# Optimization experiments

Measured on AMD Instinct MI355X. Metric: run time of the kernel, lower is better.

## Reference

```python
import jax, jax.numpy as jnp
import numpy as np

N = 50000
DIM_IN = 256
HID = 64
OUT = 32
E1 = 800000
E2 = 1600000
BN_EPS = 1e-5


def _make_edges(rng, n, e):
    row = rng.integers(0, n, size=e).astype(np.int32)
    col = rng.integers(0, n, size=e).astype(np.int32)
    # gcn_norm without self loops: val = d^{-1/2}[row] * d^{-1/2}[col]
    deg = np.bincount(row, minlength=n) + 0.0
    deg_c = np.bincount(col, minlength=n) + 0.0
    dr = 1.0 / np.sqrt(np.maximum(deg, 1.0))
    dc = 1.0 / np.sqrt(np.maximum(deg_c, 1.0))
    val = (dr[row] * dc[col]).astype(np.float32)
    return row, col, val


def setup_inputs() -> dict:
    key = jax.random.key(0)
    ks = jax.random.split(key, 4)
    rng = np.random.default_rng(0)
    e1_row, e1_col, e1_val = _make_edges(rng, N, E1)
    e2_row, e2_col, e2_val = _make_edges(rng, N, E2)
    return {
        "x": jax.random.normal(ks[0], (N, DIM_IN), dtype=jnp.float32),
        "e1_row": jnp.asarray(e1_row), "e1_col": jnp.asarray(e1_col), "e1_val": jnp.asarray(e1_val),
        "e2_row": jnp.asarray(e2_row), "e2_col": jnp.asarray(e2_col), "e2_val": jnp.asarray(e2_val),
        "W_embed": jax.random.normal(ks[1], (DIM_IN, HID), dtype=jnp.float32) * (1.0 / np.sqrt(DIM_IN)),
        "b_embed": jnp.zeros((HID,), dtype=jnp.float32),
        "bn0_gamma": jnp.ones((2 * HID,), dtype=jnp.float32),
        "bn0_beta": jnp.zeros((2 * HID,), dtype=jnp.float32),
        "bn1_gamma": jnp.ones((4 * HID,), dtype=jnp.float32),
        "bn1_beta": jnp.zeros((4 * HID,), dtype=jnp.float32),
        "W_head": jax.random.normal(ks[2], (15 * HID, OUT), dtype=jnp.float32) * (1.0 / np.sqrt(15 * HID)),
        "b_head": jnp.zeros((OUT,), dtype=jnp.float32),
    }


def _spmm(row, col, val, x, n):
    # out[row] += val * x[col]  (sparse [n,n] @ dense [n,d])
    return jax.ops.segment_sum(val[:, None] * x[col], row, num_segments=n)


def _bn(v, gamma, beta):
    # BatchNorm1d training-mode math: per-feature mean / biased var over nodes
    m = jnp.mean(v, axis=0)
    var = jnp.mean(jnp.square(v - m), axis=0)
    return gamma * (v - m) * jax.lax.rsqrt(var + BN_EPS) + beta


def reference(x, e1_row, e1_col, e1_val, e2_row, e2_col, e2_val,
              W_embed, b_embed, bn0_gamma, bn0_beta, bn1_gamma, bn1_beta,
              W_head, b_head):
    n = x.shape[0]

    def conv(h):
        h1 = _spmm(e1_row, e1_col, e1_val, h, n)
        h2 = _spmm(e2_row, e2_col, e2_val, h, n)
        return jnp.concatenate([h1, h2], axis=1)

    h = jax.nn.relu(x @ W_embed + b_embed)          # [n, HID]
    xs = [h]
    c0 = _bn(conv(h), bn0_gamma, bn0_beta)           # [n, 2*HID]
    xs.append(c0)
    c1 = _bn(conv(c0), bn1_gamma, bn1_beta)          # [n, 4*HID]
    xs.append(c1)
    c2 = conv(c1)                                    # [n, 8*HID]
    xs.append(c2)
    j = jnp.concatenate(xs, axis=1)                  # [n, 15*HID]
    return j @ W_head + b_head                       # [n, OUT]
```

## Files before the change

### kernel.cpp

```cpp
#include <hip/hip_runtime.h>


#define NN  50000
#define E1N 800000
#define E2N 1600000
#define LD  960
#define NT  3125
#define NBKT 391
#define CHUNK 8192
#define G1B 98
#define G2B 196

typedef short bf16x8 __attribute__((ext_vector_type(8)));
typedef float f32x4  __attribute__((ext_vector_type(4)));
typedef float f32x2  __attribute__((ext_vector_type(2)));

__device__ __forceinline__ float bfl(unsigned int w) { return __uint_as_float(w << 16); }
__device__ __forceinline__ float bfh(unsigned int w) { return __uint_as_float(w & 0xFFFF0000u); }
__device__ __forceinline__ float bf2f(unsigned short u) { return __uint_as_float(((unsigned int)u) << 16); }
__device__ __forceinline__ unsigned short f2bf(float f) {
    unsigned int u = __float_as_uint(f);
    u += 0x7FFFu + ((u >> 16) & 1u);
    return (unsigned short)(u >> 16);
}
__device__ __forceinline__ unsigned int pack2(float a, float b) {
    return (unsigned int)f2bf(a) | ((unsigned int)f2bf(b) << 16);
}
__device__ __forceinline__ unsigned int packfp8(float a, float b, float c, float d) {
    int w = __builtin_amdgcn_cvt_pk_fp8_f32(a, b, 0, false);
    w     = __builtin_amdgcn_cvt_pk_fp8_f32(c, d, w, true);
    return (unsigned int)w;
}
__device__ __forceinline__ f32x2 pkfma(f32x2 a, f32x2 b, f32x2 c) {
#if __has_builtin(__builtin_elementwise_fma)
    return __builtin_elementwise_fma(a, b, c);
#else
    return (f32x2){fmaf(a[0], b[0], c[0]), fmaf(a[1], b[1], c[1])};
#endif
}
__device__ __forceinline__ f32x2 bf2(unsigned int w) {
    return (f32x2){bfl(w), bfh(w)};
}


__global__ __launch_bounds__(256) void zero_kernel(float* c, int nc) {
    int i = blockIdx.x * 256 + threadIdx.x;
    if (i < nc) c[i] = 0.f;
}

__global__ __launch_bounds__(256) void bucket_count_kernel(const int* __restrict__ r1,
                                                           const int* __restrict__ r2,
                                                           int* __restrict__ bc1, int* __restrict__ bc2) {
    __shared__ int cnt[NBKT];
    for (int t = threadIdx.x; t < NBKT; t += 256) cnt[t] = 0;
    __syncthreads();
    int blk = blockIdx.x;
    const int* r; int base, lim; int* bc;
    if (blk < G1B) { r = r1; base = blk * CHUNK; lim = min(base + CHUNK, E1N); bc = bc1 + blk * NBKT; }
    else { int b2 = blk - G1B; r = r2; base = b2 * CHUNK; lim = min(base + CHUNK, E2N); bc = bc2 + b2 * NBKT; }
    for (int i = base + threadIdx.x; i < lim; i += 256)
        atomicAdd(&cnt[r[i] >> 7], 1);
    __syncthreads();
    for (int t = threadIdx.x; t < NBKT; t += 256) bc[t] = cnt[t];
}

__global__ __launch_bounds__(512) void bucket_scan_kernel(int* __restrict__ bc1, int* __restrict__ bc2) {
    __shared__ int s[512];
    int t = threadIdx.x;
    int tot1 = 0, tot2 = 0;
    if (t < NBKT) {
        for (int b = 0; b < G1B; b++) tot1 += bc1[b * NBKT + t];
        for (int b = 0; b < G2B; b++) tot2 += bc2[b * NBKT + t];
    }
    s[t] = (t < NBKT) ? tot1 : 0;
    __syncthreads();
    for (int off = 1; off < 512; off <<= 1) {
        int v = (t >= off) ? s[t - off] : 0;
        __syncthreads(); s[t] += v; __syncthreads();
    }
    int base1 = ((t < NBKT) ? s[t] : 0) - tot1;
    __syncthreads();
    s[t] = (t < NBKT) ? tot2 : 0;
    __syncthreads();
    for (int off = 1; off < 512; off <<= 1) {
        int v = (t >= off) ? s[t - off] : 0;
        __syncthreads(); s[t] += v; __syncthreads();
    }
    int base2 = ((t < NBKT) ? s[t] : 0) - tot2;
    if (t < NBKT) {
        int run = base1;
        for (int b = 0; b < G1B; b++) { int v = bc1[b * NBKT + t]; bc1[b * NBKT + t] = run; run += v; }
        run = base2;
        for (int b = 0; b < G2B; b++) { int v = bc2[b * NBKT + t]; bc2[b * NBKT + t] = run; run += v; }
    }
}

__global__ __launch_bounds__(256) void bucket_place_kernel(
        const int* __restrict__ r1, const int* __restrict__ c1, const float* __restrict__ v1,
        const int* __restrict__ r2, const int* __restrict__ c2, const float* __restrict__ v2,
        const int* __restrict__ bc1, const int* __restrict__ bc2,
        uint2* __restrict__ T1, uint2* __restrict__ T2) {
    __shared__ int pos[NBKT];
    int blk = blockIdx.x;
    const int *r, *c; const float* v; int base, lim; const int* bc; uint2* T;
    if (blk < G1B) { r = r1; c = c1; v = v1; base = blk * CHUNK; lim = min(base + CHUNK, E1N);
                     bc = bc1 + blk * NBKT; T = T1; }
    else { int b2 = blk - G1B; r = r2; c = c2; v = v2; base = b2 * CHUNK; lim = min(base + CHUNK, E2N);
           bc = bc2 + b2 * NBKT; T = T2; }
    for (int t = threadIdx.x; t < NBKT; t += 256) pos[t] = bc[t];
    __syncthreads();
    for (int i = base + threadIdx.x; i < lim; i += 256) {
        int row = r[i];
        int p = atomicAdd(&pos[row >> 7], 1);
        T[p] = make_uint2(((unsigned)c[i] << 16) | (unsigned)row, __float_as_uint(v[i]));
    }
}

__global__ __launch_bounds__(256) void bucket_sort_kernel(
        const int* __restrict__ bb1, const uint2* __restrict__ T1, int* __restrict__ rp1, unsigned int* __restrict__ Ed1,
        const int* __restrict__ bb2, const uint2* __restrict__ T2, int* __restrict__ rp2, unsigned int* __restrict__ Ed2) {
    int b = blockIdx.x % NBKT;
    int g = blockIdx.x / NBKT;
    const int* bb = g ? bb2 : bb1;
    const uint2* T = g ? T2 : T1;
    int* rp = g ? rp2 : rp1;
    unsigned int* Ed = g ? Ed2 : Ed1;
    int EN = g ? E2N : E1N;
    int beg = bb[b];
    int end = (b == NBKT - 1) ? EN : bb[b + 1];
    int R0 = b * 128;
    int nrows = min(128, NN - R0);
    __shared__ int cnt[129];
    __shared__ int cur[128];
    for (int t = threadIdx.x; t < 129; t += 256) cnt[t] = 0;
    __syncthreads();
    for (int i = beg + threadIdx.x; i < end; i += 256)
        atomicAdd(&cnt[((T[i].x & 0xFFFFu) & 127) + 1], 1);
    __syncthreads();
    for (int off = 1; off < 129; off <<= 1) {
        int v = 0;
        if (threadIdx.x < 129 && (int)threadIdx.x >= off) v = cnt[threadIdx.x - off];
        __syncthreads();
        if (threadIdx.x < 129) cnt[threadIdx.x] += v;
        __syncthreads();
    }
    if ((int)threadIdx.x < nrows) {
        int p = beg + cnt[threadIdx.x];
        cur[threadIdx.x] = p;
        rp[R0 + threadIdx.x] = p;
    }
    if (b == NBKT - 1 && threadIdx.x == 0) rp[NN] = end;
    __syncthreads();
    for (int i = beg + threadIdx.x; i < end; i += 256) {
        uint2 rec = T[i];
        int rl = (rec.x & 0xFFFFu) & 127;
        int p = atomicAdd(&cur[rl], 1);
        Ed[p] = (rec.x & 0xFFFF0000u) | (unsigned)f2bf(__uint_as_float(rec.y));
    }
}

__global__ __launch_bounds__(256) void packw_kernel(const float* __restrict__ W, unsigned short* __restrict__ Wb,
                                                    int NC, int kbs, int total) {
    int i = blockIdx.x * 256 + threadIdx.x;
    if (i >= total) return;
    int lane  = i & 63;
    int kb    = (i >> 6) % kbs;
    int ctile = i / (kbs * 64);
    int n  = ctile * 16 + (lane & 15);
    int k0 = kb * 32 + (lane >> 4) * 8;
    unsigned short v[8];
    #pragma unroll
    for (int j = 0; j < 8; j++) v[j] = f2bf(W[(k0 + j) * NC + n]);
    *(uint4*)(Wb + (size_t)i * 8) = *(uint4*)v;
}

__global__ __launch_bounds__(256) void embed_mfma_kernel(const float* __restrict__ x,
                                                         const unsigned short* __restrict__ Wb,
                                                         const float* __restrict__ bias,
                                                         unsigned short* __restrict__ Jh) {
    int wave = threadIdx.x >> 6;
    int lane = threadIdx.x & 63;
    int tile = blockIdx.x * 4 + wave;
    if (tile >= NT) return;
    int m = lane & 15;
    int q = lane >> 4;
    const float* xr = x + (size_t)(tile * 16 + m) * 256 + q * 8;
    const unsigned short* bbase = Wb + (size_t)lane * 8;
    f32x4 acc[4];
    #pragma unroll
    for (int ct = 0; ct < 4; ct++) acc[ct] = (f32x4){0.f, 0.f, 0.f, 0.f};
    #pragma unroll
    for (int kb = 0; kb < 8; kb++) {
        float4 xa = *(const float4*)(xr + kb * 32);
        float4 xb = *(const float4*)(xr + kb * 32 + 4);
        unsigned short av[8];
        av[0] = f2bf(xa.x); av[1] = f2bf(xa.y); av[2] = f2bf(xa.z); av[3] = f2bf(xa.w);
        av[4] = f2bf(xb.x); av[5] = f2bf(xb.y); av[6] = f2bf(xb.z); av[7] = f2bf(xb.w);
        bf16x8 a = *(bf16x8*)av;
        #pragma unroll
        for (int ct = 0; ct < 4; ct++) {
            bf16x8 bfr = *(const bf16x8*)(bbase + (size_t)(ct * 8 + kb) * 512);
            acc[ct] = __builtin_amdgcn_mfma_f32_16x16x32_bf16(a, bfr, acc[ct], 0, 0, 0);
        }
    }
    #pragma unroll
    for (int ct = 0; ct < 4; ct++) {
        int col = ct * 16 + m;
        float bb = bias[col];
        #pragma unroll
        for (int r = 0; r < 4; r++) {
            float v = fmaxf(acc[ct][r] + bb, 0.f);
            Jh[(size_t)(tile * 16 + q * 4 + r) * LD + col] = f2bf(v);
        }
    }
}

template <int LPR>
__global__ __launch_bounds__(256) void spmm_bf16x8_kernel(
        const int* __restrict__ rp1, const unsigned int* __restrict__ ed1,
        const int* __restrict__ rp2, const unsigned int* __restrict__ ed2,
        const unsigned short* __restrict__ src, unsigned short* __restrict__ dst) {
    constexpr int ROWS = 64 / LPR;
    constexpr int SRCF = LPR * 8;
    constexpr int RPB  = ROWS * 4;
    constexpr int GB   = (NN + RPB - 1) / RPB;
    int g    = (blockIdx.x >= GB) ? 1 : 0;
    int bx   = blockIdx.x - g * GB;
    int wave = threadIdx.x >> 6;
    int lane = threadIdx.x & 63;
    int grp  = lane / LPR;
    int sub  = lane % LPR;
    int row  = (bx * 4 + wave) * ROWS + grp;
    const int*          rp = g ? rp2 : rp1;
    const unsigned int* ed = g ? ed2 : ed1;
    bool ok = row < NN;
    int beg = 0, end = 0;
    if (ok) { beg = rp[row]; end = rp[row + 1]; }

    f32x2 acc[4];
    #pragma unroll
    for (int u = 0; u < 4; u++) acc[u] = (f32x2){0.f, 0.f};
    const unsigned short* sbase = src + sub * 8;

    int j = beg;
    for (; j + 8 <= end; j += 8) {
        unsigned int e[8];
        #pragma unroll
        for (int u = 0; u < 8; u++) e[u] = ed[j + u];
        uint4 s[8];
        #pragma unroll
        for (int u = 0; u < 8; u++) s[u] = *(const uint4*)(sbase + (size_t)(e[u] >> 16) * LD);
        #pragma unroll
        for (int u = 0; u < 8; u++) {
            float v = bfl(e[u]);
            f32x2 vv = (f32x2){v, v};
            acc[0] = pkfma(vv, bf2(s[u].x), acc[0]);
            acc[1] = pkfma(vv, bf2(s[u].y), acc[1]);
            acc[2] = pkfma(vv, bf2(s[u].z), acc[2]);
            acc[3] = pkfma(vv, bf2(s[u].w), acc[3]);
        }
    }
    for (; j < end; j++) {
        unsigned int e = ed[j];
        float v = bfl(e);
        f32x2 vv = (f32x2){v, v};
        uint4 s = *(const uint4*)(sbase + (size_t)(e >> 16) * LD);
        acc[0] = pkfma(vv, bf2(s.x), acc[0]);
        acc[1] = pkfma(vv, bf2(s.y), acc[1]);
        acc[2] = pkfma(vv, bf2(s.z), acc[2]);
        acc[3] = pkfma(vv, bf2(s.w), acc[3]);
    }

    if (ok) {
        unsigned short* dp = dst + (size_t)row * LD + g * SRCF + sub * 8;
        uint4 o;
        o.x = pack2(acc[0][0], acc[0][1]); o.y = pack2(acc[1][0], acc[1][1]);
        o.z = pack2(acc[2][0], acc[2][1]); o.w = pack2(acc[3][0], acc[3][1]);
        *(uint4*)dp = o;
    }
}

template <int LPR>
__global__ __launch_bounds__(256) void spmm_fp8x16_kernel(
        const int* __restrict__ rp1, const unsigned int* __restrict__ ed1,
        const int* __restrict__ rp2, const unsigned int* __restrict__ ed2,
        const unsigned char* __restrict__ src8,
        unsigned short* __restrict__ dst) {
    constexpr int ROWS = 64 / LPR;
    constexpr int SRCF = LPR * 16;
    constexpr int RPB  = ROWS * 4;
    constexpr int GB   = (NN + RPB - 1) / RPB;
    int g    = (blockIdx.x >= GB) ? 1 : 0;
    int bx   = blockIdx.x - g * GB;
    int wave = threadIdx.x >> 6;
    int lane = threadIdx.x & 63;
    int grp  = lane / LPR;
    int sub  = lane % LPR;
    int row  = (bx * 4 + wave) * ROWS + grp;
    const int*          rp = g ? rp2 : rp1;
    const unsigned int* ed = g ? ed2 : ed1;
    bool ok = row < NN;
    int beg = 0, end = 0;
    if (ok) { beg = rp[row]; end = rp[row + 1]; }

    f32x2 acc[8];
    #pragma unroll
    for (int u = 0; u < 8; u++) acc[u] = (f32x2){0.f, 0.f};
    const unsigned char* sbase = src8 + sub * 16;

    int j = beg;
    for (; j + 8 <= end; j += 8) {
        unsigned int e[8];
        #pragma unroll
        for (int u = 0; u < 8; u++) e[u] = ed[j + u];
        uint4 s[8];
        #pragma unroll
        for (int u = 0; u < 8; u++) s[u] = *(const uint4*)(sbase + (size_t)(e[u] >> 16) * SRCF);
        #pragma unroll
        for (int u = 0; u < 8; u++) {
            float v = bfl(e[u]);
            f32x2 vv = (f32x2){v, v};
            acc[0] = pkfma(vv, __builtin_amdgcn_cvt_pk_f32_fp8(s[u].x, false), acc[0]);
            acc[1] = pkfma(vv, __builtin_amdgcn_cvt_pk_f32_fp8(s[u].x, true),  acc[1]);
            acc[2] = pkfma(vv, __builtin_amdgcn_cvt_pk_f32_fp8(s[u].y, false), acc[2]);
            acc[3] = pkfma(vv, __builtin_amdgcn_cvt_pk_f32_fp8(s[u].y, true),  acc[3]);
            acc[4] = pkfma(vv, __builtin_amdgcn_cvt_pk_f32_fp8(s[u].z, false), acc[4]);
            acc[5] = pkfma(vv, __builtin_amdgcn_cvt_pk_f32_fp8(s[u].z, true),  acc[5]);
            acc[6] = pkfma(vv, __builtin_amdgcn_cvt_pk_f32_fp8(s[u].w, false), acc[6]);
            acc[7] = pkfma(vv, __builtin_amdgcn_cvt_pk_f32_fp8(s[u].w, true),  acc[7]);
        }
    }
    for (; j < end; j++) {
        unsigned int e = ed[j];
        float v = bfl(e);
        f32x2 vv = (f32x2){v, v};
        uint4 s = *(const uint4*)(sbase + (size_t)(e >> 16) * SRCF);
        acc[0] = pkfma(vv, __builtin_amdgcn_cvt_pk_f32_fp8(s.x, false), acc[0]);
        acc[1] = pkfma(vv, __builtin_amdgcn_cvt_pk_f32_fp8(s.x, true),  acc[1]);
        acc[2] = pkfma(vv, __builtin_amdgcn_cvt_pk_f32_fp8(s.y, false), acc[2]);
        acc[3] = pkfma(vv, __builtin_amdgcn_cvt_pk_f32_fp8(s.y, true),  acc[3]);
        acc[4] = pkfma(vv, __builtin_amdgcn_cvt_pk_f32_fp8(s.z, false), acc[4]);
        acc[5] = pkfma(vv, __builtin_amdgcn_cvt_pk_f32_fp8(s.z, true),  acc[5]);
        acc[6] = pkfma(vv, __builtin_amdgcn_cvt_pk_f32_fp8(s.w, false), acc[6]);
        acc[7] = pkfma(vv, __builtin_amdgcn_cvt_pk_f32_fp8(s.w, true),  acc[7]);
    }

    if (ok) {
        unsigned short* dp = dst + (size_t)row * LD + g * SRCF + sub * 16;
        uint4 o1, o2;
        o1.x = pack2(acc[0][0], acc[0][1]); o1.y = pack2(acc[1][0], acc[1][1]);
        o1.z = pack2(acc[2][0], acc[2][1]); o1.w = pack2(acc[3][0], acc[3][1]);
        o2.x = pack2(acc[4][0], acc[4][1]); o2.y = pack2(acc[5][0], acc[5][1]);
        o2.z = pack2(acc[6][0], acc[6][1]); o2.w = pack2(acc[7][0], acc[7][1]);
        *(uint4*)dp = o1;
        *(uint4*)(dp + 8) = o2;
    }
}

template <int F>
__global__ __launch_bounds__(256) void bn_stats_kernel(const unsigned short* __restrict__ c,
                                                       float* sum, float* sumsq) {
    constexpr int SL = 256 / F;
    int f  = threadIdx.x % F;
    int sl = threadIdx.x / F;
    float s = 0.f, ss = 0.f;
    for (int r = blockIdx.x * SL + sl; r < NN; r += gridDim.x * SL) {
        float v = bf2f(c[(size_t)r * LD + f]);
        s += v; ss += v * v;
    }
    __shared__ float ls[256], lss[256];
    ls[threadIdx.x] = s; lss[threadIdx.x] = ss;
    __syncthreads();
    if (sl == 0) {
        #pragma unroll
        for (int u = 1; u < SL; u++) { s += ls[f + u * F]; ss += lss[f + u * F]; }
        atomicAdd(&sum[f], s);
        atomicAdd(&sumsq[f], ss);
    }
}

__global__ void bn_finalize_kernel(const float* sum, const float* sumsq, const float* __restrict__ gamma,
                                   const float* __restrict__ beta, float* scale, float* shift, int F) {
    int f = blockIdx.x * blockDim.x + threadIdx.x;
    if (f >= F) return;
    float m   = sum[f] * (1.0f / NN);
    float var = sumsq[f] * (1.0f / NN) - m * m;
    float sc  = gamma[f] * rsqrtf(var + 1e-5f);
    scale[f] = sc;
    shift[f] = beta[f] - m * sc;
}

template <int F>
__global__ __launch_bounds__(256) void bn_apply_kernel(unsigned short* __restrict__ c,
                                                       const float* __restrict__ scale,
                                                       const float* __restrict__ shift) {
    constexpr int FV = F / 4;
    int idx  = blockIdx.x * 256 + threadIdx.x;
    int node = idx / FV;
    int fo   = (idx % FV) * 4;
    if (node >= NN) return;
    unsigned short* p = c + (size_t)node * LD + fo;
    uint2 v = *(uint2*)p;
    float a0 = bfl(v.x), a1 = bfh(v.x), a2 = bfl(v.y), a3 = bfh(v.y);
    float4 sc = *(const float4*)(scale + fo);
    float4 sh = *(const float4*)(shift + fo);
    a0 = fmaf(a0, sc.x, sh.x);
    a1 = fmaf(a1, sc.y, sh.y);
    a2 = fmaf(a2, sc.z, sh.z);
    a3 = fmaf(a3, sc.w, sh.w);
    v.x = pack2(a0, a1); v.y = pack2(a2, a3);
    *(uint2*)p = v;
}

__global__ __launch_bounds__(256) void bn_apply_fp8_kernel(unsigned short* __restrict__ c,
                                                           unsigned char* __restrict__ c8,
                                                           const float* __restrict__ scale,
                                                           const float* __restrict__ shift) {
    int idx  = blockIdx.x * 256 + threadIdx.x;
    int node = idx >> 6;
    int fo   = (idx & 63) * 4;
    if (node >= NN) return;
    unsigned short* p = c + (size_t)node * LD + fo;
    uint2 v = *(uint2*)p;
    float a0 = bfl(v.x), a1 = bfh(v.x), a2 = bfl(v.y), a3 = bfh(v.y);
    float4 sc = *(const float4*)(scale + fo);
    float4 sh = *(const float4*)(shift + fo);
    a0 = fmaf(a0, sc.x, sh.x);
    a1 = fmaf(a1, sc.y, sh.y);
    a2 = fmaf(a2, sc.z, sh.z);
    a3 = fmaf(a3, sc.w, sh.w);
    v.x = pack2(a0, a1); v.y = pack2(a2, a3);
    *(uint2*)p = v;
    *(unsigned int*)(c8 + (size_t)node * 256 + fo) = packfp8(a0, a1, a2, a3);
}

__global__ __launch_bounds__(256) void head_mfma_kernel(const unsigned short* __restrict__ Jh,
                                                        const unsigned short* __restrict__ Wb,
                                                        const float* __restrict__ b,
                                                        float* __restrict__ out) {
    int wave = threadIdx.x >> 6;
    int lane = threadIdx.x & 63;
    int tile = blockIdx.x * 4 + wave;
    if (tile >= NT) return;
    int m = lane & 15;
    int q = lane >> 4;
    const unsigned short* arow  = Jh + (size_t)(tile * 16 + m) * LD + q * 8;
    const unsigned short* bbase = Wb + (size_t)lane * 8;
    f32x4 acc0 = {0.f, 0.f, 0.f, 0.f};
    f32x4 acc1 = {0.f, 0.f, 0.f, 0.f};
    #pragma unroll 5
    for (int kb = 0; kb < 30; kb++) {
        bf16x8 a  = *(const bf16x8*)(arow + kb * 32);
        bf16x8 b0 = *(const bf16x8*)(bbase + (size_t)kb * 512);
        bf16x8 b1 = *(const bf16x8*)(bbase + (size_t)(30 + kb) * 512);
        acc0 = __builtin_amdgcn_mfma_f32_16x16x32_bf16(a, b0, acc0, 0, 0, 0);
        acc1 = __builtin_amdgcn_mfma_f32_16x16x32_bf16(a, b1, acc1, 0, 0, 0);
    }
    int col = m;
    float b0 = b[col], b1 = b[16 + col];
    #pragma unroll
    for (int r = 0; r < 4; r++) {
        float* op = out + (size_t)(tile * 16 + q * 4 + r) * 32 + col;
        op[0]  = acc0[r] + b0;
        op[16] = acc1[r] + b1;
    }
}


extern "C" void kernel_launch(void* const* d_in, const int* in_sizes, int n_in,
                              void* d_out, int out_size, void* d_ws, size_t ws_size,
                              hipStream_t stream) {
    const float* x      = (const float*)d_in[0];
    const int*   e1_row = (const int*)d_in[1];
    const int*   e1_col = (const int*)d_in[2];
    const float* e1_val = (const float*)d_in[3];
    const int*   e2_row = (const int*)d_in[4];
    const int*   e2_col = (const int*)d_in[5];
    const float* e2_val = (const float*)d_in[6];
    const float* W_emb  = (const float*)d_in[7];
    const float* b_emb  = (const float*)d_in[8];
    const float* bn0_g  = (const float*)d_in[9];
    const float* bn0_b  = (const float*)d_in[10];
    const float* bn1_g  = (const float*)d_in[11];
    const float* bn1_b  = (const float*)d_in[12];
    const float* W_head = (const float*)d_in[13];
    const float* b_head = (const float*)d_in[14];
    float* out = (float*)d_out;

    char* ws = (char*)d_ws;
    auto alloc = [&](size_t bytes) -> char* {
        char* p = ws;
        ws += (bytes + 255) & ~(size_t)255;
        return p;
    };
    int*   rp1   = (int*)alloc((NN + 1) * 4);
    int*   rp2   = (int*)alloc((NN + 1) * 4);
    int*   bc1   = (int*)alloc((size_t)G1B * NBKT * 4);
    int*   bc2   = (int*)alloc((size_t)G2B * NBKT * 4);
    unsigned int* Ed1 = (unsigned int*)alloc((size_t)E1N * 4);
    unsigned int* Ed2 = (unsigned int*)alloc((size_t)E2N * 4);
    float* stats = (float*)alloc(1536 * 4);
    unsigned short* Wbh  = (unsigned short*)alloc(3840 * 8 * 2);
    unsigned short* Wbe  = (unsigned short*)alloc(2048 * 8 * 2);
    unsigned char*  C1f8 = (unsigned char*)alloc((size_t)NN * 256);
    unsigned short* Jh   = (unsigned short*)alloc((size_t)NN * LD * 2);
    uint2* T1 = (uint2*)Jh;
    uint2* T2 = T1 + E1N;

    float* sum0   = stats;        float* sq0    = stats + 128;
    float* sum1   = stats + 256;  float* sq1    = stats + 512;
    float* scale0 = stats + 768;  float* shift0 = stats + 896;
    float* scale1 = stats + 1024; float* shift1 = stats + 1280;

    zero_kernel<<<3, 256, 0, stream>>>(stats, 768);
    bucket_count_kernel<<<G1B + G2B, 256, 0, stream>>>(e1_row, e2_row, bc1, bc2);
    bucket_scan_kernel<<<1, 512, 0, stream>>>(bc1, bc2);
    bucket_place_kernel<<<G1B + G2B, 256, 0, stream>>>(e1_row, e1_col, e1_val,
                                                       e2_row, e2_col, e2_val, bc1, bc2, T1, T2);
    bucket_sort_kernel<<<2 * NBKT, 256, 0, stream>>>(bc1, T1, rp1, Ed1, bc2, T2, rp2, Ed2);
    packw_kernel<<<15, 256, 0, stream>>>(W_head, Wbh, 32, 30, 3840);
    packw_kernel<<<8, 256, 0, stream>>>(W_emb, Wbe, 64, 8, 2048);

    embed_mfma_kernel<<<(NT + 3) / 4, 256, 0, stream>>>(x, Wbe, b_emb, Jh);

    spmm_bf16x8_kernel<8><<<2 * ((NN + 31) / 32), 256, 0, stream>>>(rp1, Ed1, rp2, Ed2, Jh, Jh + 64);
    bn_stats_kernel<128><<<512, 256, 0, stream>>>(Jh + 64, sum0, sq0);
    bn_finalize_kernel<<<1, 128, 0, stream>>>(sum0, sq0, bn0_g, bn0_b, scale0, shift0, 128);
    bn_apply_kernel<128><<<(NN * 32 + 255) / 256, 256, 0, stream>>>(Jh + 64, scale0, shift0);

    spmm_bf16x8_kernel<16><<<2 * (NN / 16), 256, 0, stream>>>(rp1, Ed1, rp2, Ed2, Jh + 64, Jh + 192);
    bn_stats_kernel<256><<<512, 256, 0, stream>>>(Jh + 192, sum1, sq1);
    bn_finalize_kernel<<<1, 256, 0, stream>>>(sum1, sq1, bn1_g, bn1_b, scale1, shift1, 256);
    bn_apply_fp8_kernel<<<(NN * 64 + 255) / 256, 256, 0, stream>>>(Jh + 192, C1f8, scale1, shift1);

    spmm_fp8x16_kernel<16><<<2 * (NN / 16), 256, 0, stream>>>(rp1, Ed1, rp2, Ed2, C1f8, Jh + 448);

    head_mfma_kernel<<<(NT + 3) / 4, 256, 0, stream>>>(Jh, Wbh, b_head, out);
}
```

Baseline: 543.7 us.

## Slice SpMM feature columns across XCDs so each die caches a source slice

The three SpMM kernels are restructured so that each block handles 64 rows but only a 32-column (bf16) or 64-byte (fp8) feature slice. Block indices are mapped so that each XCD always works on the same feature slice, which keeps the gathered source working set per XCD's L2 smaller. The edge lists are re-read once per slice. Edge loads and output stores also become nontemporal to avoid polluting cache with streaming data. The trade-off is duplicated edge-index traffic and row-pointer reads across slices.

```diff
diff --git a/kernel.cpp b/kernel.cpp
--- a/kernel.cpp
+++ b/kernel.cpp
@@ -10,10 +10,12 @@
 #define CHUNK 8192
 #define G1B 98
 #define G2B 196
+#define RG  782
 
 typedef short bf16x8 __attribute__((ext_vector_type(8)));
 typedef float f32x4  __attribute__((ext_vector_type(4)));
 typedef float f32x2  __attribute__((ext_vector_type(2)));
+typedef unsigned int u32x4 __attribute__((ext_vector_type(4)));
 
 __device__ __forceinline__ float bfl(unsigned int w) { return __uint_as_float(w << 16); }
 __device__ __forceinline__ float bfh(unsigned int w) { return __uint_as_float(w & 0xFFFF0000u); }
@@ -215,22 +217,23 @@
     }
 }
 
-template <int LPR>
-__global__ __launch_bounds__(256) void spmm_bf16x8_kernel(
+template <int NSL>
+__global__ __launch_bounds__(256) void spmm_bf16_sliced_kernel(
         const int* __restrict__ rp1, const unsigned int* __restrict__ ed1,
         const int* __restrict__ rp2, const unsigned int* __restrict__ ed2,
         const unsigned short* __restrict__ src, unsigned short* __restrict__ dst) {
-    constexpr int ROWS = 64 / LPR;
-    constexpr int SRCF = LPR * 8;
-    constexpr int RPB  = ROWS * 4;
-    constexpr int GB   = (NN + RPB - 1) / RPB;
-    int g    = (blockIdx.x >= GB) ? 1 : 0;
-    int bx   = blockIdx.x - g * GB;
-    int wave = threadIdx.x >> 6;
-    int lane = threadIdx.x & 63;
-    int grp  = lane / LPR;
-    int sub  = lane % LPR;
-    int row  = (bx * 4 + wave) * ROWS + grp;
+    constexpr int XPS = 8 / NSL;
+    int bid   = blockIdx.x;
+    int xcd   = bid & 7;
+    int slice = xcd / XPS;
+    int idx   = (bid >> 3) * XPS + (xcd % XPS);
+    int g     = (idx >= RG) ? 1 : 0;
+    int bx    = idx - g * RG;
+    int wave  = threadIdx.x >> 6;
+    int lane  = threadIdx.x & 63;
+    int grp   = lane >> 2;
+    int sub   = lane & 3;
+    int row   = bx * 64 + wave * 16 + grp;
     const int*          rp = g ? rp2 : rp1;
     const unsigned int* ed = g ? ed2 : ed1;
     bool ok = row < NN;
@@ -240,13 +243,13 @@
     f32x2 acc[4];
     #pragma unroll
     for (int u = 0; u < 4; u++) acc[u] = (f32x2){0.f, 0.f};
-    const unsigned short* sbase = src + sub * 8;
+    const unsigned short* sbase = src + slice * 32 + sub * 8;
 
     int j = beg;
     for (; j + 8 <= end; j += 8) {
         unsigned int e[8];
         #pragma unroll
-        for (int u = 0; u < 8; u++) e[u] = ed[j + u];
+        for (int u = 0; u < 8; u++) e[u] = __builtin_nontemporal_load(ed + j + u);
         uint4 s[8];
         #pragma unroll
         for (int u = 0; u < 8; u++) s[u] = *(const uint4*)(sbase + (size_t)(e[u] >> 16) * LD);
@@ -261,7 +264,7 @@
         }
     }
     for (; j < end; j++) {
-        unsigned int e = ed[j];
+        unsigned int e = __builtin_nontemporal_load(ed + j);
         float v = bfl(e);
         f32x2 vv = (f32x2){v, v};
         uint4 s = *(const uint4*)(sbase + (size_t)(e >> 16) * LD);
@@ -272,31 +275,30 @@
     }
 
     if (ok) {
-        unsigned short* dp = dst + (size_t)row * LD + g * SRCF + sub * 8;
-        uint4 o;
+        unsigned short* dp = dst + (size_t)row * LD + g * (NSL * 32) + slice * 32 + sub * 8;
+        u32x4 o;
         o.x = pack2(acc[0][0], acc[0][1]); o.y = pack2(acc[1][0], acc[1][1]);
         o.z = pack2(acc[2][0], acc[2][1]); o.w = pack2(acc[3][0], acc[3][1]);
-        *(uint4*)dp = o;
-    }
-}
-
-template <int LPR>
-__global__ __launch_bounds__(256) void spmm_fp8x16_kernel(
+        __builtin_nontemporal_store(o, (u32x4*)dp);
+    }
+}
+
+__global__ __launch_bounds__(256) void spmm_fp8_sliced_kernel(
         const int* __restrict__ rp1, const unsigned int* __restrict__ ed1,
         const int* __restrict__ rp2, const unsigned int* __restrict__ ed2,
         const unsigned char* __restrict__ src8,
         unsigned short* __restrict__ dst) {
-    constexpr int ROWS = 64 / LPR;
-    constexpr int SRCF = LPR * 16;
-    constexpr int RPB  = ROWS * 4;
-    constexpr int GB   = (NN + RPB - 1) / RPB;
-    int g    = (blockIdx.x >= GB) ? 1 : 0;
-    int bx   = blockIdx.x - g * GB;
-    int wave = threadIdx.x >> 6;
-    int lane = threadIdx.x & 63;
-    int grp  = lane / LPR;
-    int sub  = lane % LPR;
-    int row  = (bx * 4 + wave) * ROWS + grp;
+    int bid   = blockIdx.x;
+    int xcd   = bid & 7;
+    int slice = xcd >> 1;
+    int idx   = (bid >> 3) * 2 + (xcd & 1);
+    int g     = (idx >= RG) ? 1 : 0;
+    int bx    = idx - g * RG;
+    int wave  = threadIdx.x >> 6;
+    int lane  = threadIdx.x & 63;
+    int grp   = lane >> 2;
+    int sub   = lane & 3;
+    int row   = bx * 64 + wave * 16 + grp;
     const int*          rp = g ? rp2 : rp1;
     const unsigned int* ed = g ? ed2 : ed1;
     bool ok = row < NN;
@@ -306,16 +308,16 @@
     f32x2 acc[8];
     #pragma unroll
     for (int u = 0; u < 8; u++) acc[u] = (f32x2){0.f, 0.f};
-    const unsigned char* sbase = src8 + sub * 16;
+    const unsigned char* sbase = src8 + slice * 64 + sub * 16;
 
     int j = beg;
     for (; j + 8 <= end; j += 8) {
         unsigned int e[8];
         #pragma unroll
-        for (int u = 0; u < 8; u++) e[u] = ed[j + u];
+        for (int u = 0; u < 8; u++) e[u] = __builtin_nontemporal_load(ed + j + u);
         uint4 s[8];
         #pragma unroll
-        for (int u = 0; u < 8; u++) s[u] = *(const uint4*)(sbase + (size_t)(e[u] >> 16) * SRCF);
+        for (int u = 0; u < 8; u++) s[u] = *(const uint4*)(sbase + (size_t)(e[u] >> 16) * 256);
         #pragma unroll
         for (int u = 0; u < 8; u++) {
             float v = bfl(e[u]);
@@ -331,10 +333,10 @@
         }
     }
     for (; j < end; j++) {
-        unsigned int e = ed[j];
+        unsigned int e = __builtin_nontemporal_load(ed + j);
         float v = bfl(e);
         f32x2 vv = (f32x2){v, v};
-        uint4 s = *(const uint4*)(sbase + (size_t)(e >> 16) * SRCF);
+        uint4 s = *(const uint4*)(sbase + (size_t)(e >> 16) * 256);
         acc[0] = pkfma(vv, __builtin_amdgcn_cvt_pk_f32_fp8(s.x, false), acc[0]);
         acc[1] = pkfma(vv, __builtin_amdgcn_cvt_pk_f32_fp8(s.x, true),  acc[1]);
         acc[2] = pkfma(vv, __builtin_amdgcn_cvt_pk_f32_fp8(s.y, false), acc[2]);
@@ -346,14 +348,14 @@
     }
 
     if (ok) {
-        unsigned short* dp = dst + (size_t)row * LD + g * SRCF + sub * 16;
-        uint4 o1, o2;
+        unsigned short* dp = dst + (size_t)row * LD + g * 256 + slice * 64 + sub * 16;
+        u32x4 o1, o2;
         o1.x = pack2(acc[0][0], acc[0][1]); o1.y = pack2(acc[1][0], acc[1][1]);
         o1.z = pack2(acc[2][0], acc[2][1]); o1.w = pack2(acc[3][0], acc[3][1]);
         o2.x = pack2(acc[4][0], acc[4][1]); o2.y = pack2(acc[5][0], acc[5][1]);
         o2.z = pack2(acc[6][0], acc[6][1]); o2.w = pack2(acc[7][0], acc[7][1]);
-        *(uint4*)dp = o1;
-        *(uint4*)(dp + 8) = o2;
+        __builtin_nontemporal_store(o1, (u32x4*)dp);
+        __builtin_nontemporal_store(o2, (u32x4*)(dp + 8));
     }
 }
 
@@ -523,17 +525,17 @@
 
     embed_mfma_kernel<<<(NT + 3) / 4, 256, 0, stream>>>(x, Wbe, b_emb, Jh);
 
-    spmm_bf16x8_kernel<8><<<2 * ((NN + 31) / 32), 256, 0, stream>>>(rp1, Ed1, rp2, Ed2, Jh, Jh + 64);
+    spmm_bf16_sliced_kernel<2><<<8 * ((2 * RG) / 4), 256, 0, stream>>>(rp1, Ed1, rp2, Ed2, Jh, Jh + 64);
     bn_stats_kernel<128><<<512, 256, 0, stream>>>(Jh + 64, sum0, sq0);
     bn_finalize_kernel<<<1, 128, 0, stream>>>(sum0, sq0, bn0_g, bn0_b, scale0, shift0, 128);
     bn_apply_kernel<128><<<(NN * 32 + 255) / 256, 256, 0, stream>>>(Jh + 64, scale0, shift0);
 
-    spmm_bf16x8_kernel<16><<<2 * (NN / 16), 256, 0, stream>>>(rp1, Ed1, rp2, Ed2, Jh + 64, Jh + 192);
+    spmm_bf16_sliced_kernel<4><<<8 * ((2 * RG) / 2), 256, 0, stream>>>(rp1, Ed1, rp2, Ed2, Jh + 64, Jh + 192);
     bn_stats_kernel<256><<<512, 256, 0, stream>>>(Jh + 192, sum1, sq1);
     bn_finalize_kernel<<<1, 256, 0, stream>>>(sum1, sq1, bn1_g, bn1_b, scale1, shift1, 256);
     bn_apply_fp8_kernel<<<(NN * 64 + 255) / 256, 256, 0, stream>>>(Jh + 192, C1f8, scale1, shift1);
 
-    spmm_fp8x16_kernel<16><<<2 * (NN / 16), 256, 0, stream>>>(rp1, Ed1, rp2, Ed2, C1f8, Jh + 448);
+    spmm_fp8_sliced_kernel<<<8 * ((2 * RG) / 2), 256, 0, stream>>>(rp1, Ed1, rp2, Ed2, C1f8, Jh + 448);
 
     head_mfma_kernel<<<(NT + 3) / 4, 256, 0, stream>>>(Jh, Wbh, b_head, out);
 }
```

New measurement: 720.4 us. 32.5% more time.
